# Optimization experiments

Hardware: AMD Instinct MI355X
Metric: run time of the kernel (lower is better)

## Reference

```python
import jax, jax.numpy as jnp
import numpy as np

B_T, NF, C = 2048, 128, 256  # batch*time, num_freq_bins, in_channels
LN_EPS = 1e-5


def _build_expert_prior(nf, sr=16000, fmin=0, fmax=8000, tol=0.2):
    # Faithful port of _build_expert_knowledge_prior (mel-spaced centers,
    mel_min = 2595 * np.log10(1 + fmin / 700)
    mel_max = 2595 * np.log10(1 + fmax / 700)
    mels = np.linspace(mel_min, mel_max, nf)
    cf = 700 * (10 ** (mels / 2595) - 1)
    A = np.zeros((nf, nf), dtype=np.float64)
    for i in range(nf):
        for j in range(nf):
            if i == j:
                A[i, j] = 1.0
                continue
            if abs(i - j) == 1:
                A[i, j] = max(A[i, j], 0.3)
                A[j, i] = max(A[j, i], 0.3)
            ratio = cf[j] / (cf[i] + 1e-8)
            for k in (2.0, 3.0, 4.0):
                if abs(ratio - k) < tol:
                    A[i, j] = max(A[i, j], np.exp(-(ratio - k) ** 2 / 0.1 ** 2))
                    A[j, i] = A[i, j]
    A = A / (A.sum(axis=1, keepdims=True) + 1e-8)
    return jnp.asarray(A, dtype=jnp.float32)


def setup_inputs() -> dict:
    key = jax.random.key(0)
    ks = jax.random.split(key, 12)
    s_in = 1.0 / np.sqrt(C)
    return {
        "x": jax.random.normal(ks[0], (B_T, NF, C), jnp.float32),
        "entity_embedding": jax.random.normal(ks[1], (1, NF, C), jnp.float32),
        "knowledge_adj": _build_expert_prior(NF),
        "fallback_alpha": jnp.array([0.5], jnp.float32),
        "Wq": jax.random.normal(ks[2], (C // 2, C), jnp.float32) * s_in,
        "bq": jax.random.normal(ks[3], (C // 2,), jnp.float32) * 0.01,
        "Wk": jax.random.normal(ks[4], (C // 2, C), jnp.float32) * s_in,
        "bk": jax.random.normal(ks[5], (C // 2,), jnp.float32) * 0.01,
        "Wv": jax.random.normal(ks[6], (C, C), jnp.float32) * s_in,
        "bv": jax.random.normal(ks[7], (C,), jnp.float32) * 0.01,
        "Wg": jax.random.normal(ks[8], (C, C), jnp.float32) * s_in,
        "bg": jax.random.normal(ks[9], (C,), jnp.float32) * 0.01,
        "gamma": jnp.ones((C,), jnp.float32),
        "beta": jnp.zeros((C,), jnp.float32),
    }


def reference(x, entity_embedding, knowledge_adj, fallback_alpha,
              Wq, bq, Wk, bk, Wv, bv, Wg, bg, gamma, beta):
    xe = x + entity_embedding                       # [B_T, NF, C]
    Q = xe @ Wq.T + bq                              # [B_T, NF, C/2]
    K = xe @ Wk.T + bk                              # [B_T, NF, C/2]
    V = x @ Wv.T + bv                               # [B_T, NF, C]
    scale = jnp.sqrt(jnp.asarray(Q.shape[-1], x.dtype))
    scores = jnp.einsum('bnd,bmd->bnm', Q, K) / scale   # [B_T, NF, NF]
    # additive knowledge-graph bias (fallback_alpha path, broadcast over batch)
    scores = scores + fallback_alpha[0] * jax.nn.relu(knowledge_adj)
    attn = jax.nn.softmax(scores, axis=-1)          # dropout = identity (eval)
    z = jnp.einsum('bnm,bmc->bnc', attn, V)         # GCN-style AV aggregation
    z = z @ Wg.T + bg
    h = x + jax.nn.relu(z)                          # residual
    mu = jnp.mean(h, axis=-1, keepdims=True)        # LayerNorm over C
    var = jnp.mean(jnp.square(h - mu), axis=-1, keepdims=True)
    return (h - mu) * jax.lax.rsqrt(var + LN_EPS) * gamma + beta
```

## Files before the change

kernel.cpp:

```cpp
#include <hip/hip_runtime.h>

typedef short short8 __attribute__((ext_vector_type(8)));
typedef float f32x4  __attribute__((ext_vector_type(4)));

#define NFQ 128
#define CH  256

__device__ __forceinline__ unsigned short f2bf(float f) {
  unsigned u = __float_as_uint(f);
  u += 0x7fffu + ((u >> 16) & 1u);
  return (unsigned short)(u >> 16);
}
__device__ __forceinline__ float bf2f(unsigned short h) {
  return __uint_as_float(((unsigned)h) << 16);
}

__global__ void akg_prep(const float* __restrict__ Wg,
                         const float* __restrict__ Wv,
                         const float* __restrict__ bv,
                         const float* __restrict__ bg,
                         const float* __restrict__ adj,
                         const float* __restrict__ alpha,
                         const float* __restrict__ Wq,
                         const float* __restrict__ Wk,
                         unsigned short* __restrict__ wf,
                         float* __restrict__ bfull,
                         float* __restrict__ biasf,
                         unsigned short* __restrict__ wqb,
                         unsigned short* __restrict__ wkb) {
  int blk = blockIdx.x, t = threadIdx.x;
  if (blk < 256) {
    float acc = 0.f;
    for (int j = 0; j < 256; j++)
      acc += Wg[blk*256 + j] * Wv[j*256 + t];
    wf[blk*256 + t] = f2bf(acc);
  } else if (blk == 256) {
    float acc = bg[t];
    for (int j = 0; j < 256; j++)
      acc += Wg[t*256 + j] * bv[j];
    bfull[t] = acc;
  } else if (blk == 257) {
    float a = alpha[0];
    for (int i = t; i < 128*128; i += 256)
      biasf[i] = a * fmaxf(adj[i], 0.f);
  } else if (blk == 258) {
    for (int i = t; i < 128*256; i += 256) wqb[i] = f2bf(Wq[i]);
  } else {
    for (int i = t; i < 128*256; i += 256) wkb[i] = f2bf(Wk[i]);
  }
}

__global__ __launch_bounds__(512, 2) void akg_main(
    const float* __restrict__ x,
    const float* __restrict__ ent,
    const unsigned short* __restrict__ wqb,
    const float* __restrict__ bq,
    const unsigned short* __restrict__ wkb,
    const float* __restrict__ bk,
    const unsigned short* __restrict__ wf,
    const float* __restrict__ bfull,
    const float* __restrict__ biasf,
    const float* __restrict__ gma,
    const float* __restrict__ bta,
    float* __restrict__ out) {
  const int b    = blockIdx.x;
  const int t    = threadIdx.x;
  const int wv   = t >> 6;
  const int lane = t & 63;
  const int q    = lane >> 4;
  const int l16  = lane & 15;
  const int rw   = wv * 16;

  __shared__ __align__(16) unsigned short S[69632];
  unsigned short* Ks = S;
  unsigned short* Qs = S + 17408;
  unsigned short* Vt = S + 34816;
  unsigned short* Hs = S;

  const float* xb = x + (size_t)b * NFQ * CH;
  const int arow = rw + l16;
  const f32x4 zero4 = {0.f, 0.f, 0.f, 0.f};

  short8 xf[8];
#pragma unroll
  for (int ks = 0; ks < 8; ks++) {
    f32x4 a0 = *(const f32x4*)(xb + arow*CH + ks*32 + q*8);
    f32x4 a1 = *(const f32x4*)(xb + arow*CH + ks*32 + q*8 + 4);
    short8 s;
#pragma unroll
    for (int j = 0; j < 4; j++) {
      s[j]     = (short)f2bf(a0[j]);
      s[4 + j] = (short)f2bf(a1[j]);
    }
    xf[ks] = s;
  }

  f32x4 av[16];
#pragma unroll
  for (int nt = 0; nt < 16; nt++) av[nt] = zero4;
#pragma unroll
  for (int ks = 0; ks < 8; ks++) {
#pragma unroll
    for (int nt = 0; nt < 16; nt++) {
      short8 bf = *(const short8*)(wf + (nt*16 + l16)*CH + ks*32 + q*8);
      av[nt] = __builtin_amdgcn_mfma_f32_16x16x32_bf16(xf[ks], bf, av[nt], 0, 0, 0);
    }
  }
#pragma unroll
  for (int nt = 0; nt < 16; nt++) {
    float bfc = bfull[nt*16 + l16];
    unsigned p0 = (unsigned)f2bf(av[nt][0] + bfc) | ((unsigned)f2bf(av[nt][1] + bfc) << 16);
    unsigned p1 = (unsigned)f2bf(av[nt][2] + bfc) | ((unsigned)f2bf(av[nt][3] + bfc) << 16);
    uint2 pk; pk.x = p0; pk.y = p1;
    *(uint2*)(Vt + (nt*16 + l16)*136 + rw + q*4) = pk;
  }

#pragma unroll
  for (int ks = 0; ks < 8; ks++) {
    f32x4 e0 = *(const f32x4*)(ent + arow*CH + ks*32 + q*8);
    f32x4 e1 = *(const f32x4*)(ent + arow*CH + ks*32 + q*8 + 4);
#pragma unroll
    for (int j = 0; j < 4; j++) {
      xf[ks][j]     = (short)f2bf(bf2f((unsigned short)xf[ks][j])     + e0[j]);
      xf[ks][4 + j] = (short)f2bf(bf2f((unsigned short)xf[ks][4 + j]) + e1[j]);
    }
  }

  f32x4 ac[8];
#pragma unroll
  for (int nt = 0; nt < 8; nt++) ac[nt] = zero4;
#pragma unroll
  for (int ks = 0; ks < 8; ks++) {
#pragma unroll
    for (int nt = 0; nt < 8; nt++) {
      short8 bf = *(const short8*)(wkb + (nt*16 + l16)*CH + ks*32 + q*8);
      ac[nt] = __builtin_amdgcn_mfma_f32_16x16x32_bf16(xf[ks], bf, ac[nt], 0, 0, 0);
    }
  }
#pragma unroll
  for (int nt = 0; nt < 8; nt++) {
    float bb = bk[nt*16 + l16];
#pragma unroll
    for (int r = 0; r < 4; r++)
      Ks[(rw + q*4 + r)*136 + nt*16 + l16] = f2bf(ac[nt][r] + bb);
  }

#pragma unroll
  for (int nt = 0; nt < 8; nt++) ac[nt] = zero4;
#pragma unroll
  for (int ks = 0; ks < 8; ks++) {
#pragma unroll
    for (int nt = 0; nt < 8; nt++) {
      short8 bf = *(const short8*)(wqb + (nt*16 + l16)*CH + ks*32 + q*8);
      ac[nt] = __builtin_amdgcn_mfma_f32_16x16x32_bf16(xf[ks], bf, ac[nt], 0, 0, 0);
    }
  }
  const float RS = 0.08838834764831845f;
#pragma unroll
  for (int nt = 0; nt < 8; nt++) {
    float bb = bq[nt*16 + l16];
#pragma unroll
    for (int r = 0; r < 4; r++)
      Qs[(rw + q*4 + r)*136 + nt*16 + l16] = f2bf((ac[nt][r] + bb) * RS);
  }

  __syncthreads();

#pragma unroll
  for (int nt = 0; nt < 8; nt++) ac[nt] = zero4;
#pragma unroll
  for (int ks = 0; ks < 4; ks++) {
    short8 af = *(const short8*)(Qs + (rw + l16)*136 + ks*32 + q*8);
#pragma unroll
    for (int nt = 0; nt < 8; nt++) {
      short8 bf = *(const short8*)(Ks + (nt*16 + l16)*136 + ks*32 + q*8);
      ac[nt] = __builtin_amdgcn_mfma_f32_16x16x32_bf16(af, bf, ac[nt], 0, 0, 0);
    }
  }
#pragma unroll
  for (int nt = 0; nt < 8; nt++)
#pragma unroll
    for (int r = 0; r < 4; r++)
      ac[nt][r] += biasf[(rw + q*4 + r)*128 + nt*16 + l16];

  float inv[4];
#pragma unroll
  for (int r = 0; r < 4; r++) {
    float mx = -1e30f;
#pragma unroll
    for (int nt = 0; nt < 8; nt++) mx = fmaxf(mx, ac[nt][r]);
    mx = fmaxf(mx, __shfl_xor(mx, 1));
    mx = fmaxf(mx, __shfl_xor(mx, 2));
    mx = fmaxf(mx, __shfl_xor(mx, 4));
    mx = fmaxf(mx, __shfl_xor(mx, 8));
    float s = 0.f;
#pragma unroll
    for (int nt = 0; nt < 8; nt++) {
      float e = __expf(ac[nt][r] - mx);
      ac[nt][r] = e; s += e;
    }
    s += __shfl_xor(s, 1);
    s += __shfl_xor(s, 2);
    s += __shfl_xor(s, 4);
    s += __shfl_xor(s, 8);
    inv[r] = 1.f / s;
  }
#pragma unroll
  for (int nt = 0; nt < 8; nt++)
#pragma unroll
    for (int r = 0; r < 4; r++)
      Qs[(rw + q*4 + r)*136 + nt*16 + l16] = f2bf(ac[nt][r] * inv[r]);

#pragma unroll
  for (int nt = 0; nt < 16; nt++) av[nt] = zero4;
#pragma unroll
  for (int ks = 0; ks < 4; ks++) {
    short8 af = *(const short8*)(Qs + (rw + l16)*136 + ks*32 + q*8);
#pragma unroll
    for (int nt = 0; nt < 16; nt++) {
      short8 bf = *(const short8*)(Vt + (nt*16 + l16)*136 + ks*32 + q*8);
      av[nt] = __builtin_amdgcn_mfma_f32_16x16x32_bf16(af, bf, av[nt], 0, 0, 0);
    }
  }

  __syncthreads();

#pragma unroll
  for (int nt = 0; nt < 16; nt++)
#pragma unroll
    for (int r = 0; r < 4; r++)
      Hs[(rw + q*4 + r)*264 + nt*16 + l16] = f2bf(fmaxf(av[nt][r], 0.f));

  __syncthreads();

  {
    const int row = t >> 2;
    const int seg = t & 3;
    const float* xrow = xb + row*CH + seg*64;
    float hv[64];
    float sum = 0.f, ss = 0.f;
#pragma unroll
    for (int i = 0; i < 8; i++) {
      short8 hz = *(const short8*)(Hs + row*264 + seg*64 + i*8);
      f32x4 x0 = *(const f32x4*)(xrow + i*8);
      f32x4 x1 = *(const f32x4*)(xrow + i*8 + 4);
#pragma unroll
      for (int j = 0; j < 4; j++) {
        float v0 = x0[j] + bf2f((unsigned short)hz[j]);
        float v1 = x1[j] + bf2f((unsigned short)hz[4 + j]);
        hv[i*8 + j]     = v0;
        hv[i*8 + 4 + j] = v1;
        sum += v0 + v1; ss += v0*v0 + v1*v1;
      }
    }
    sum += __shfl_xor(sum, 1); sum += __shfl_xor(sum, 2);
    ss  += __shfl_xor(ss , 1); ss  += __shfl_xor(ss , 2);
    float mean = sum * (1.f/256.f);
    float var  = ss * (1.f/256.f) - mean*mean;
    float rstd = rsqrtf(var + 1e-5f);
    float* ob = out + (size_t)b * NFQ * CH + row*CH + seg*64;
#pragma unroll
    for (int i = 0; i < 8; i++) {
      f32x4 g0 = *(const f32x4*)(gma + seg*64 + i*8);
      f32x4 g1 = *(const f32x4*)(gma + seg*64 + i*8 + 4);
      f32x4 b0 = *(const f32x4*)(bta + seg*64 + i*8);
      f32x4 b1 = *(const f32x4*)(bta + seg*64 + i*8 + 4);
      f32x4 o0, o1;
#pragma unroll
      for (int j = 0; j < 4; j++) {
        o0[j] = (hv[i*8 + j]     - mean) * rstd * g0[j] + b0[j];
        o1[j] = (hv[i*8 + 4 + j] - mean) * rstd * g1[j] + b1[j];
      }
      *(f32x4*)(ob + i*8)     = o0;
      *(f32x4*)(ob + i*8 + 4) = o1;
    }
  }
}

extern "C" void kernel_launch(void* const* d_in, const int* in_sizes, int n_in,
                              void* d_out, int out_size, void* d_ws, size_t ws_size,
                              hipStream_t stream) {
  const float* x     = (const float*)d_in[0];
  const float* ent   = (const float*)d_in[1];
  const float* adj   = (const float*)d_in[2];
  const float* alpha = (const float*)d_in[3];
  const float* Wq    = (const float*)d_in[4];
  const float* bq    = (const float*)d_in[5];
  const float* Wk    = (const float*)d_in[6];
  const float* bk    = (const float*)d_in[7];
  const float* Wv    = (const float*)d_in[8];
  const float* bv    = (const float*)d_in[9];
  const float* Wg    = (const float*)d_in[10];
  const float* bg    = (const float*)d_in[11];
  const float* gma   = (const float*)d_in[12];
  const float* bta   = (const float*)d_in[13];

  unsigned short* wf    = (unsigned short*)d_ws;
  float*          bfull = (float*)((char*)d_ws + 131072);
  float*          biasf = (float*)((char*)d_ws + 132096);
  unsigned short* wqb   = (unsigned short*)((char*)d_ws + 197632);
  unsigned short* wkb   = (unsigned short*)((char*)d_ws + 263168);

  float* out = (float*)d_out;

  akg_prep<<<260, 256, 0, stream>>>(Wg, Wv, bv, bg, adj, alpha, Wq, Wk,
                                    wf, bfull, biasf, wqb, wkb);
  akg_main<<<2048, 512, 0, stream>>>(x, ent, wqb, bq, wkb, bk, wf, bfull, biasf,
                                     gma, bta, out);
}
```

Measured before the change: 1.089 ms.

## Split V projection into two halves to halve LDS and raise occupancy

The fused V projection and attention-times-V product now run in two 128-channel halves that reuse the K buffer region, so the separate V-transpose LDS buffer goes away. Shared memory per block is halved and launch bounds are raised from 2 to 4 blocks per CU. x is reloaded from global and converted to bf16 again after the Q/K stage, and ent is added to x in fp32 before rounding rather than after. The cost is extra barriers, a second read of x, and register pressure that must now fit the tighter launch bound. There is also an unroll pragma on the prep kernel's dot loops.

Result: slower. 1.166 ms (+7.0%).

```diff
diff --git a/kernel.cpp b/kernel.cpp
--- a/kernel.cpp
+++ b/kernel.cpp
@@ -31,11 +31,13 @@
   int blk = blockIdx.x, t = threadIdx.x;
   if (blk < 256) {
     float acc = 0.f;
+#pragma unroll 8
     for (int j = 0; j < 256; j++)
       acc += Wg[blk*256 + j] * Wv[j*256 + t];
     wf[blk*256 + t] = f2bf(acc);
   } else if (blk == 256) {
     float acc = bg[t];
+#pragma unroll 8
     for (int j = 0; j < 256; j++)
       acc += Wg[t*256 + j] * bv[j];
     bfull[t] = acc;
@@ -50,7 +52,7 @@
   }
 }
 
-__global__ __launch_bounds__(512, 2) void akg_main(
+__global__ __launch_bounds__(512, 4) void akg_main(
     const float* __restrict__ x,
     const float* __restrict__ ent,
     const unsigned short* __restrict__ wqb,
@@ -71,10 +73,9 @@
   const int l16  = lane & 15;
   const int rw   = wv * 16;
 
-  __shared__ __align__(16) unsigned short S[69632];
-  unsigned short* Ks = S;
-  unsigned short* Qs = S + 17408;
-  unsigned short* Vt = S + 34816;
+  __shared__ __align__(16) unsigned short S[34816];
+  unsigned short* Qs = S;
+  unsigned short* Ks = S + 17408;
   unsigned short* Hs = S;
 
   const float* xb = x + (size_t)b * NFQ * CH;
@@ -86,44 +87,15 @@
   for (int ks = 0; ks < 8; ks++) {
     f32x4 a0 = *(const f32x4*)(xb + arow*CH + ks*32 + q*8);
     f32x4 a1 = *(const f32x4*)(xb + arow*CH + ks*32 + q*8 + 4);
-    short8 s;
-#pragma unroll
-    for (int j = 0; j < 4; j++) {
-      s[j]     = (short)f2bf(a0[j]);
-      s[4 + j] = (short)f2bf(a1[j]);
-    }
-    xf[ks] = s;
-  }
-
-  f32x4 av[16];
-#pragma unroll
-  for (int nt = 0; nt < 16; nt++) av[nt] = zero4;
-#pragma unroll
-  for (int ks = 0; ks < 8; ks++) {
-#pragma unroll
-    for (int nt = 0; nt < 16; nt++) {
-      short8 bf = *(const short8*)(wf + (nt*16 + l16)*CH + ks*32 + q*8);
-      av[nt] = __builtin_amdgcn_mfma_f32_16x16x32_bf16(xf[ks], bf, av[nt], 0, 0, 0);
-    }
-  }
-#pragma unroll
-  for (int nt = 0; nt < 16; nt++) {
-    float bfc = bfull[nt*16 + l16];
-    unsigned p0 = (unsigned)f2bf(av[nt][0] + bfc) | ((unsigned)f2bf(av[nt][1] + bfc) << 16);
-    unsigned p1 = (unsigned)f2bf(av[nt][2] + bfc) | ((unsigned)f2bf(av[nt][3] + bfc) << 16);
-    uint2 pk; pk.x = p0; pk.y = p1;
-    *(uint2*)(Vt + (nt*16 + l16)*136 + rw + q*4) = pk;
-  }
-
-#pragma unroll
-  for (int ks = 0; ks < 8; ks++) {
     f32x4 e0 = *(const f32x4*)(ent + arow*CH + ks*32 + q*8);
     f32x4 e1 = *(const f32x4*)(ent + arow*CH + ks*32 + q*8 + 4);
+    short8 s;
 #pragma unroll
     for (int j = 0; j < 4; j++) {
-      xf[ks][j]     = (short)f2bf(bf2f((unsigned short)xf[ks][j])     + e0[j]);
-      xf[ks][4 + j] = (short)f2bf(bf2f((unsigned short)xf[ks][4 + j]) + e1[j]);
-    }
+      s[j]     = (short)f2bf(a0[j] + e0[j]);
+      s[4 + j] = (short)f2bf(a1[j] + e1[j]);
+    }
+    xf[ks] = s;
   }
 
   f32x4 ac[8];
@@ -212,24 +184,127 @@
       Qs[(rw + q*4 + r)*136 + nt*16 + l16] = f2bf(ac[nt][r] * inv[r]);
 
 #pragma unroll
-  for (int nt = 0; nt < 16; nt++) av[nt] = zero4;
-#pragma unroll
-  for (int ks = 0; ks < 4; ks++) {
-    short8 af = *(const short8*)(Qs + (rw + l16)*136 + ks*32 + q*8);
-#pragma unroll
-    for (int nt = 0; nt < 16; nt++) {
-      short8 bf = *(const short8*)(Vt + (nt*16 + l16)*136 + ks*32 + q*8);
-      av[nt] = __builtin_amdgcn_mfma_f32_16x16x32_bf16(af, bf, av[nt], 0, 0, 0);
-    }
-  }
-
-  __syncthreads();
-
-#pragma unroll
-  for (int nt = 0; nt < 16; nt++)
-#pragma unroll
-    for (int r = 0; r < 4; r++)
-      Hs[(rw + q*4 + r)*264 + nt*16 + l16] = f2bf(fmaxf(av[nt][r], 0.f));
+  for (int ks = 0; ks < 8; ks++) {
+    f32x4 a0 = *(const f32x4*)(xb + arow*CH + ks*32 + q*8);
+    f32x4 a1 = *(const f32x4*)(xb + arow*CH + ks*32 + q*8 + 4);
+    short8 s;
+#pragma unroll
+    for (int j = 0; j < 4; j++) {
+      s[j]     = (short)f2bf(a0[j]);
+      s[4 + j] = (short)f2bf(a1[j]);
+    }
+    xf[ks] = s;
+  }
+
+  __syncthreads();
+
+  uint2 h1[8], h2[8];
+
+  {
+    f32x4 vc[8];
+#pragma unroll
+    for (int nt = 0; nt < 8; nt++) vc[nt] = zero4;
+#pragma unroll
+    for (int ks = 0; ks < 8; ks++) {
+#pragma unroll
+      for (int nt = 0; nt < 8; nt++) {
+        short8 bf = *(const short8*)(wf + (nt*16 + l16)*CH + ks*32 + q*8);
+        vc[nt] = __builtin_amdgcn_mfma_f32_16x16x32_bf16(xf[ks], bf, vc[nt], 0, 0, 0);
+      }
+    }
+#pragma unroll
+    for (int nt = 0; nt < 8; nt++) {
+      float bfc = bfull[nt*16 + l16];
+      unsigned p0 = (unsigned)f2bf(vc[nt][0] + bfc) | ((unsigned)f2bf(vc[nt][1] + bfc) << 16);
+      unsigned p1 = (unsigned)f2bf(vc[nt][2] + bfc) | ((unsigned)f2bf(vc[nt][3] + bfc) << 16);
+      uint2 pk; pk.x = p0; pk.y = p1;
+      *(uint2*)(Ks + (nt*16 + l16)*136 + rw + q*4) = pk;
+    }
+  }
+  __syncthreads();
+
+  {
+    f32x4 av[8];
+#pragma unroll
+    for (int nt = 0; nt < 8; nt++) av[nt] = zero4;
+#pragma unroll
+    for (int ks = 0; ks < 4; ks++) {
+      short8 af = *(const short8*)(Qs + (rw + l16)*136 + ks*32 + q*8);
+#pragma unroll
+      for (int nt = 0; nt < 8; nt++) {
+        short8 bf = *(const short8*)(Ks + (nt*16 + l16)*136 + ks*32 + q*8);
+        av[nt] = __builtin_amdgcn_mfma_f32_16x16x32_bf16(af, bf, av[nt], 0, 0, 0);
+      }
+    }
+#pragma unroll
+    for (int nt = 0; nt < 8; nt++) {
+      h1[nt].x = (unsigned)f2bf(fmaxf(av[nt][0], 0.f)) |
+                 ((unsigned)f2bf(fmaxf(av[nt][1], 0.f)) << 16);
+      h1[nt].y = (unsigned)f2bf(fmaxf(av[nt][2], 0.f)) |
+                 ((unsigned)f2bf(fmaxf(av[nt][3], 0.f)) << 16);
+    }
+  }
+  __syncthreads();
+
+  {
+    f32x4 vc[8];
+#pragma unroll
+    for (int nt = 0; nt < 8; nt++) vc[nt] = zero4;
+#pragma unroll
+    for (int ks = 0; ks < 8; ks++) {
+#pragma unroll
+      for (int nt = 0; nt < 8; nt++) {
+        short8 bf = *(const short8*)(wf + ((nt + 8)*16 + l16)*CH + ks*32 + q*8);
+        vc[nt] = __builtin_amdgcn_mfma_f32_16x16x32_bf16(xf[ks], bf, vc[nt], 0, 0, 0);
+      }
+    }
+#pragma unroll
+    for (int nt = 0; nt < 8; nt++) {
+      float bfc = bfull[(nt + 8)*16 + l16];
+      unsigned p0 = (unsigned)f2bf(vc[nt][0] + bfc) | ((unsigned)f2bf(vc[nt][1] + bfc) << 16);
+      unsigned p1 = (unsigned)f2bf(vc[nt][2] + bfc) | ((unsigned)f2bf(vc[nt][3] + bfc) << 16);
+      uint2 pk; pk.x = p0; pk.y = p1;
+      *(uint2*)(Ks + (nt*16 + l16)*136 + rw + q*4) = pk;
+    }
+  }
+  __syncthreads();
+
+  {
+    f32x4 av[8];
+#pragma unroll
+    for (int nt = 0; nt < 8; nt++) av[nt] = zero4;
+#pragma unroll
+    for (int ks = 0; ks < 4; ks++) {
+      short8 af = *(const short8*)(Qs + (rw + l16)*136 + ks*32 + q*8);
+#pragma unroll
+      for (int nt = 0; nt < 8; nt++) {
+        short8 bf = *(const short8*)(Ks + (nt*16 + l16)*136 + ks*32 + q*8);
+        av[nt] = __builtin_amdgcn_mfma_f32_16x16x32_bf16(af, bf, av[nt], 0, 0, 0);
+      }
+    }
+#pragma unroll
+    for (int nt = 0; nt < 8; nt++) {
+      h2[nt].x = (unsigned)f2bf(fmaxf(av[nt][0], 0.f)) |
+                 ((unsigned)f2bf(fmaxf(av[nt][1], 0.f)) << 16);
+      h2[nt].y = (unsigned)f2bf(fmaxf(av[nt][2], 0.f)) |
+                 ((unsigned)f2bf(fmaxf(av[nt][3], 0.f)) << 16);
+    }
+  }
+
+  __syncthreads();
+
+#pragma unroll
+  for (int nt = 0; nt < 8; nt++) {
+    const int col = nt*16 + l16;
+    Hs[(rw + q*4 + 0)*264 + col] = (unsigned short)(h1[nt].x & 0xffffu);
+    Hs[(rw + q*4 + 1)*264 + col] = (unsigned short)(h1[nt].x >> 16);
+    Hs[(rw + q*4 + 2)*264 + col] = (unsigned short)(h1[nt].y & 0xffffu);
+    Hs[(rw + q*4 + 3)*264 + col] = (unsigned short)(h1[nt].y >> 16);
+    Hs[(rw + q*4 + 0)*264 + 128 + col] = (unsigned short)(h2[nt].x & 0xffffu);
+    Hs[(rw + q*4 + 1)*264 + 128 + col] = (unsigned short)(h2[nt].x >> 16);
+    Hs[(rw + q*4 + 2)*264 + 128 + col] = (unsigned short)(h2[nt].y & 0xffffu);
+    Hs[(rw + q*4 + 3)*264 + 128 + col] = (unsigned short)(h2[nt].y >> 16);
+  }
 
   __syncthreads();
 
```
